# Kernel optimization log

Measured on AMD Instinct MI355X. Metric: run time of the kernel, lower is better.

The kernel has to match this reference:

```python
import jax, jax.numpy as jnp
import numpy as np

B, CIN, COUT, H, W, K, S = 32, 16, 32, 14, 14, 5, 2


def _conv(x, w, stride, groups=1):
    # x: [N, Cin_g*groups, H, W], w: [Cout, Cin_g, K, K], VALID padding, no bias
    return jax.lax.conv_general_dilated(
        x, w, (stride, stride), 'VALID',
        dimension_numbers=('NCHW', 'OIHW', 'NCHW'),
        feature_group_count=groups)


def setup_inputs() -> dict:
    key = jax.random.key(0)
    k1, k2, k3 = jax.random.split(key, 3)
    u = jax.random.normal(k1, (B, CIN, H, W), jnp.float32)
    C = jax.random.normal(k2, (B, CIN, H, W, H, W), jnp.float32)
    # per-output-channel single-channel kernels, as in Conv2d(1,1,K) list
    w = jax.random.normal(k3, (COUT, 1, K, K), jnp.float32) * (1.0 / K)
    return {"u": u, "C": C, "w": w}


def reference(u, C, w):
    b, cin, h, wd = u.shape
    cout = w.shape[0]
    # ---- mean path: conv each input channel with every kernel, sum over Cin ----
    m = _conv(u.reshape(b * cin, 1, h, wd), w, S)          # [b*cin, cout, OH, OW]
    oh, ow = m.shape[2], m.shape[3]
    out_mean = m.reshape(b, cin, cout, oh, ow).sum(axis=1)  # [b, cout, OH, OW]

    # ---- covariance path: apply the same conv to both spatial index pairs ----
    # conv over original dims (4,5)
    t = _conv(C.reshape(b * cin * h * wd, 1, h, wd), w, S)  # [b*cin*h*w, cout, OH, OW]
    t = t.reshape(b, cin, h, wd, cout, oh, ow)
    # bring original dims (2,3) to conv position; keep kernel index as channel
    t = t.transpose(0, 1, 5, 6, 4, 2, 3)                    # [b, cin, OH, OW, cout, h, w]
    t = t.reshape(b * cin * oh * ow, cout, h, wd)
    # grouped conv: channel i convolved with kernel i (second application)
    t = _conv(t, w, S, groups=cout)                         # [b*cin*OH*OW, cout, OH, OW]
    t = t.reshape(b, cin, oh, ow, cout, oh, ow)             # [b,c,oh45,ow45,i,oh23,ow23]
    # torch output layout: [b, i, oh23, ow23, oh45, ow45], summed over cin
    out_cov = t.transpose(0, 4, 5, 6, 2, 3, 1).sum(axis=-1)
    return (out_mean, out_cov)
```

## Files before the change

kernel.cpp:

```cpp
#include <hip/hip_runtime.h>


#define NB   32
#define NCIN 16
#define NCO  32
#define HH   14
#define OH13 13
#define SLAB 328
#define T1_PER_BI  4264
#define T1_PER_BI4 1066

__device__ float g_T1[NB * NCO * T1_PER_BI];

__global__ __launch_bounds__(448) void k1_reduce_conv(const float* __restrict__ C,
                                                      const float* __restrict__ w) {
  const int xcd  = blockIdx.x & 7;
  const int slot = blockIdx.x >> 3;
  const int b    = xcd + 8 * (slot / OH13);
  const int h1   = slot % OH13;
  const int tid  = threadIdx.x;

  __shared__ float wl[NCO * 25];
  __shared__ __align__(16) float buf[NCO * SLAB];

  for (int t = tid; t < NCO * 25; t += 448) wl[t] = w[t];

  const float4* C4 = (const float4*)C;
  const int base4 = ((b * NCIN) * HH + h1) * 686;
  for (int j4 = tid; j4 < 686; j4 += 448) {
    float4 acc = make_float4(0.f, 0.f, 0.f, 0.f);
    #pragma unroll
    for (int c = 0; c < NCIN; ++c) {
      float4 v = C4[base4 + c * 9604 + j4];
      acc.x += v.x; acc.y += v.y; acc.z += v.z; acc.w += v.w;
    }
    const float vv[4] = {acc.x, acc.y, acc.z, acc.w};
    const int j    = j4 * 4;
    const int w1   = j / 196;
    const int rem0 = j - w1 * 196;
    #pragma unroll
    for (int e = 0; e < 4; ++e) {
      const int rem = rem0 + e;
      const int h2 = rem / 14, w2 = rem - h2 * 14;
      buf[w1 * 224 + h2 * 16 + w2] = vv[e];
    }
  }
  __syncthreads();

  const int i  = tid & 31;
  const int w1 = tid >> 5;
  float wr[25];
  #pragma unroll
  for (int t = 0; t < 25; ++t) wr[t] = wl[i * 25 + t];

  float acc[25];
  #pragma unroll
  for (int t = 0; t < 25; ++t) acc[t] = 0.f;

  if (w1 < OH13) {
    #pragma unroll
    for (int r = 0; r < 5; ++r) {
      #pragma unroll
      for (int cc = 0; cc < 5; ++cc) {
        const int row = 2 * r + cc;
        const float4* rp = (const float4*)(buf + w1 * 224 + row * 16);
        float4 x0 = rp[0], x1 = rp[1], x2 = rp[2], x3 = rp[3];
        const float col[16] = {x0.x, x0.y, x0.z, x0.w,
                               x1.x, x1.y, x1.z, x1.w,
                               x2.x, x2.y, x2.z, x2.w,
                               x3.x, x3.y, x3.z, x3.w};
        #pragma unroll
        for (int s = 0; s < 5; ++s) {
          #pragma unroll
          for (int d = 0; d < 5; ++d)
            acc[r * 5 + s] += wr[cc * 5 + d] * col[2 * s + d];
        }
      }
    }
  }
  __syncthreads();

  if (w1 < OH13) {
    #pragma unroll
    for (int t = 0; t < 25; ++t) buf[i * SLAB + w1 * 25 + t] = acc[t];
  } else {
    buf[i * SLAB + 325] = 0.f;
    buf[i * SLAB + 326] = 0.f;
    buf[i * SLAB + 327] = 0.f;
  }
  __syncthreads();

  const float4* t1s4 = (const float4*)buf;
  float4* G4 = (float4*)g_T1;
  const int gbase4 = (b * NCO) * T1_PER_BI4 + h1 * 82;
  for (int idx4 = tid; idx4 < NCO * 82; idx4 += 448) {
    const int i2  = idx4 / 82;
    const int rem = idx4 - i2 * 82;
    G4[gbase4 + i2 * T1_PER_BI4 + rem] = t1s4[idx4];
  }
}

__global__ __launch_bounds__(256) void k2_out(const float* __restrict__ u,
                                              const float* __restrict__ w,
                                              float* __restrict__ out) {
  const int blk = blockIdx.x;
  const int tid = threadIdx.x;

  if (blk < NB * NCO) {
    const int xcd  = blk & 7;
    const int slot = blk >> 3;
    const int b    = xcd + 8 * (slot >> 5);
    const int i    = slot & 31;
    const int bi   = b * NCO + i;

    __shared__ __align__(16) float sl[T1_PER_BI];
    const float4* src = (const float4*)(g_T1 + (size_t)bi * T1_PER_BI);
    float4* sl4 = (float4*)sl;
    for (int j = tid; j < T1_PER_BI4; j += 256) sl4[j] = src[j];

    float wr[25];
    #pragma unroll
    for (int t = 0; t < 25; ++t) wr[t] = w[i * 25 + t];
    __syncthreads();

    for (int o = tid; o < 625; o += 256) {
      const int p  = o / 125;
      const int q  = (o / 25) % 5;
      const int rs = o % 25;
      float acc = 0.f;
      #pragma unroll
      for (int a = 0; a < 5; ++a) {
        #pragma unroll
        for (int bb = 0; bb < 5; ++bb)
          acc += wr[a * 5 + bb] * sl[(2 * p + a) * SLAB + (2 * q + bb) * 25 + rs];
      }
      out[25600 + bi * 625 + o] = acc;
    }
  } else {
    const int b = blk - NB * NCO;
    __shared__ float us[196];
    for (int j = tid; j < 196; j += 256) {
      float acc = 0.f;
      #pragma unroll
      for (int c = 0; c < NCIN; ++c) acc += u[(b * NCIN + c) * 196 + j];
      us[j] = acc;
    }
    __syncthreads();
    for (int o = tid; o < NCO * 25; o += 256) {
      const int i = o / 25;
      const int p = (o / 5) % 5;
      const int q = o % 5;
      float acc = 0.f;
      #pragma unroll
      for (int a = 0; a < 5; ++a) {
        #pragma unroll
        for (int bb = 0; bb < 5; ++bb)
          acc += w[i * 25 + a * 5 + bb] * us[(2 * p + a) * 14 + 2 * q + bb];
      }
      out[b * 800 + o] = acc;
    }
  }
}

extern "C" void kernel_launch(void* const* d_in, const int* in_sizes, int n_in,
                              void* d_out, int out_size, void* d_ws, size_t ws_size,
                              hipStream_t stream) {
  const float* u = (const float*)d_in[0];
  const float* C = (const float*)d_in[1];
  const float* w = (const float*)d_in[2];
  float* out = (float*)d_out;

  hipLaunchKernelGGL(k1_reduce_conv, dim3(8 * 52), dim3(448), 0, stream, C, w);
  hipLaunchKernelGGL(k2_out, dim3(NB * NCO + NB), dim3(256), 0, stream, u, w, out);
}
```

Baseline: 126.1 us.

## Pad intermediate rows to 28 floats, vectorize second conv, and skip unused C columns

Each row of the intermediate T1 is padded from 25 to 28 floats, so the second-stage kernel can read float4 vectors, and each thread now computes four outputs instead of one. The first kernel loads only the 13 of 14 w1 slices that the stride-2 conv actually uses, which cuts global reads of the large C tensor. Its conv loop is reordered to load each smem row once and reuse it across all kernel rows that need it. In exchange the intermediate buffer and its global traffic grow slightly, and only 175 threads per block do work in k2.

```diff
diff --git a/kernel.cpp b/kernel.cpp
--- a/kernel.cpp
+++ b/kernel.cpp
@@ -6,9 +6,10 @@
 #define NCO  32
 #define HH   14
 #define OH13 13
-#define SLAB 328
-#define T1_PER_BI  4264
-#define T1_PER_BI4 1066
+#define RS28 28
+#define SLABW 364
+#define T1_PER_BI  4732
+#define T1_PER_BI4 1183
 
 __device__ float g_T1[NB * NCO * T1_PER_BI];
 
@@ -21,27 +22,27 @@
   const int tid  = threadIdx.x;
 
   __shared__ float wl[NCO * 25];
-  __shared__ __align__(16) float buf[NCO * SLAB];
+  __shared__ __align__(16) float buf[NCO * SLABW];
 
   for (int t = tid; t < NCO * 25; t += 448) wl[t] = w[t];
 
   const float4* C4 = (const float4*)C;
   const int base4 = ((b * NCIN) * HH + h1) * 686;
-  for (int j4 = tid; j4 < 686; j4 += 448) {
+  for (int u = tid; u < 598; u += 448) {
+    const int w1 = u / 46, j = u - w1 * 46;
+    const int g  = base4 + w1 * 49 + j;
     float4 acc = make_float4(0.f, 0.f, 0.f, 0.f);
     #pragma unroll
     for (int c = 0; c < NCIN; ++c) {
-      float4 v = C4[base4 + c * 9604 + j4];
+      float4 v = C4[g + c * 9604 + 0];
       acc.x += v.x; acc.y += v.y; acc.z += v.z; acc.w += v.w;
     }
     const float vv[4] = {acc.x, acc.y, acc.z, acc.w};
-    const int j    = j4 * 4;
-    const int w1   = j / 196;
-    const int rem0 = j - w1 * 196;
+    const int jj0 = j * 4;
     #pragma unroll
     for (int e = 0; e < 4; ++e) {
-      const int rem = rem0 + e;
-      const int h2 = rem / 14, w2 = rem - h2 * 14;
+      const int jj = jj0 + e;
+      const int h2 = jj / 14, w2 = jj - h2 * 14;
       buf[w1 * 224 + h2 * 16 + w2] = vv[e];
     }
   }
@@ -59,16 +60,17 @@
 
   if (w1 < OH13) {
     #pragma unroll
-    for (int r = 0; r < 5; ++r) {
+    for (int n = 0; n < 13; ++n) {
+      const float4* rp = (const float4*)(buf + w1 * 224 + n * 16);
+      float4 x0 = rp[0], x1 = rp[1], x2 = rp[2], x3 = rp[3];
+      const float col[16] = {x0.x, x0.y, x0.z, x0.w,
+                             x1.x, x1.y, x1.z, x1.w,
+                             x2.x, x2.y, x2.z, x2.w,
+                             x3.x, x3.y, x3.z, x3.w};
       #pragma unroll
-      for (int cc = 0; cc < 5; ++cc) {
-        const int row = 2 * r + cc;
-        const float4* rp = (const float4*)(buf + w1 * 224 + row * 16);
-        float4 x0 = rp[0], x1 = rp[1], x2 = rp[2], x3 = rp[3];
-        const float col[16] = {x0.x, x0.y, x0.z, x0.w,
-                               x1.x, x1.y, x1.z, x1.w,
-                               x2.x, x2.y, x2.z, x2.w,
-                               x3.x, x3.y, x3.z, x3.w};
+      for (int r = 0; r < 5; ++r) {
+        const int cc = n - 2 * r;
+        if (cc < 0 || cc > 4) continue;
         #pragma unroll
         for (int s = 0; s < 5; ++s) {
           #pragma unroll
@@ -82,20 +84,19 @@
 
   if (w1 < OH13) {
     #pragma unroll
-    for (int t = 0; t < 25; ++t) buf[i * SLAB + w1 * 25 + t] = acc[t];
-  } else {
-    buf[i * SLAB + 325] = 0.f;
-    buf[i * SLAB + 326] = 0.f;
-    buf[i * SLAB + 327] = 0.f;
+    for (int t = 0; t < 25; ++t) buf[i * SLABW + w1 * RS28 + t] = acc[t];
+    buf[i * SLABW + w1 * RS28 + 25] = 0.f;
+    buf[i * SLABW + w1 * RS28 + 26] = 0.f;
+    buf[i * SLABW + w1 * RS28 + 27] = 0.f;
   }
   __syncthreads();
 
   const float4* t1s4 = (const float4*)buf;
   float4* G4 = (float4*)g_T1;
-  const int gbase4 = (b * NCO) * T1_PER_BI4 + h1 * 82;
-  for (int idx4 = tid; idx4 < NCO * 82; idx4 += 448) {
-    const int i2  = idx4 / 82;
-    const int rem = idx4 - i2 * 82;
+  const int gbase4 = (b * NCO) * T1_PER_BI4 + h1 * 91;
+  for (int idx4 = tid; idx4 < NCO * 91; idx4 += 448) {
+    const int i2  = idx4 / 91;
+    const int rem = idx4 - i2 * 91;
     G4[gbase4 + i2 * T1_PER_BI4 + rem] = t1s4[idx4];
   }
 }
@@ -123,18 +124,22 @@
     for (int t = 0; t < 25; ++t) wr[t] = w[i * 25 + t];
     __syncthreads();
 
-    for (int o = tid; o < 625; o += 256) {
-      const int p  = o / 125;
-      const int q  = (o / 25) % 5;
-      const int rs = o % 25;
-      float acc = 0.f;
+    if (tid < 175) {
+      const int pq = tid / 7, rs4 = tid - pq * 7;
+      const int p = pq / 5, q = pq - p * 5;
+      float4 acc = make_float4(0.f, 0.f, 0.f, 0.f);
       #pragma unroll
       for (int a = 0; a < 5; ++a) {
         #pragma unroll
-        for (int bb = 0; bb < 5; ++bb)
-          acc += wr[a * 5 + bb] * sl[(2 * p + a) * SLAB + (2 * q + bb) * 25 + rs];
+        for (int bb = 0; bb < 5; ++bb) {
+          const float4 v = *(const float4*)(sl + ((2 * p + a) * OH13 + (2 * q + bb)) * RS28 + rs4 * 4);
+          const float wv = wr[a * 5 + bb];
+          acc.x += wv * v.x; acc.y += wv * v.y; acc.z += wv * v.z; acc.w += wv * v.w;
+        }
       }
-      out[25600 + bi * 625 + o] = acc;
+      float* dst = out + 25600 + bi * 625 + pq * 25 + rs4 * 4;
+      dst[0] = acc.x;
+      if (rs4 < 6) { dst[1] = acc.y; dst[2] = acc.z; dst[3] = acc.w; }
     }
   } else {
     const int b = blk - NB * NCO;
```

New measurement: 123.3 us. 2.2% less time.
